# Performance work log

Measured on AMD Instinct MI355X. Metric: run time of the kernel, lower is better.

Reference implementation:

```python
import jax, jax.numpy as jnp
import numpy as np

MARGIN = 1.0
N, D = 4096, 512
NUM_CLASSES = 64


def setup_inputs() -> dict:
    key = jax.random.key(0)
    k1, k2 = jax.random.split(key)
    inputs = jax.random.normal(k1, (N, D), dtype=jnp.float32)
    targets = jax.random.randint(k2, (N,), 0, NUM_CLASSES, dtype=jnp.int64)
    return {"inputs": inputs, "targets": targets}


def reference(inputs, targets):
    n = inputs.shape[0]
    sq = jnp.sum(inputs * inputs, axis=1)  # [n]
    # squared Euclidean distances, clamped at 0 (matches relu in original)
    d2 = jnp.maximum(sq[:, None] + sq[None, :] - 2.0 * (inputs @ inputs.T), 0.0)
    # safe sqrt (zero entries get 0, matching forward; avoids NaN grads)
    dist = jnp.where(d2 > 0, jnp.sqrt(jnp.where(d2 > 0, d2, 1.0)), 0.0)  # [n,n]

    same = targets[:, None] == targets[None, :]
    eye = jnp.eye(n, dtype=bool)
    pos_mask = same & ~eye          # positives, diagonal excluded
    neg_mask = ~same                # negatives (diagonal is same-label, excluded)

    # per-row sum_k exp(margin - d_ik) over negatives  (replaces per-pair loop)
    neg_sum = jnp.sum(jnp.where(neg_mask, jnp.exp(MARGIN - dist), 0.0), axis=1)  # [n]

    # J_ij = log(neg_sum_i + neg_sum_j) + d_ij for positive pairs
    J = jnp.log(neg_sum[:, None] + neg_sum[None, :]) + dist
    triu_pos = jnp.triu(pos_mask)   # loop iterated over upper-triangular positives
    hinge2 = jnp.where(triu_pos, jax.nn.relu(J) ** 2, 0.0)

    # original divides by count of ALL positive entries (both triangles)
    len_p = jnp.sum(pos_mask).astype(jnp.float32)
    return jnp.sum(hinge2) / len_p
```

## Files before the change

### kernel.cpp

```cpp
#include <hip/hip_runtime.h>
#include <math.h>

#define NN 4096
#define DD 512
#define MARGINF 1.0f
#define NCLS 64
#define MAXM 160
#define TRI (MAXM * (MAXM - 1) / 2)
#define PBLK 32
#define NBLK2 (PBLK * (PBLK + 1) / 2)
#define NSLICE 4

typedef __attribute__((ext_vector_type(8))) short bf16x8;
typedef __attribute__((ext_vector_type(4))) float f32x4;

#define WS_SQ   0
#define WS_NS   4096
#define WS_LOSS 8192
#define WS_CTR  8193
#define WS_LENP 8194
#define WS_RK   8320
#define WS_MEM  12416
#define WS_XF   32768
#define WS_PD   1081344

__device__ __forceinline__ unsigned short f2bf(float f) {
    unsigned u = __float_as_uint(f);
    u += 0x7fffu + ((u >> 16) & 1u);
    return (unsigned short)(u >> 16);
}

__global__ __launch_bounds__(256) void prep_kernel(const float* __restrict__ X,
                                                   const int* __restrict__ tgt,
                                                   float* __restrict__ ws) {
    __shared__ int tg[NN];
    const int tid = threadIdx.x;
    for (int j = tid; j < NN; j += 256) tg[j] = tgt[j];

    const int wv = tid >> 6, lane = tid & 63;
    const int row = blockIdx.x * 4 + wv;
    const float4* xr = (const float4*)(X + (size_t)row * DD);
    float4 a = xr[2 * lane], b = xr[2 * lane + 1];
    float s = a.x * a.x + a.y * a.y + a.z * a.z + a.w * a.w
            + b.x * b.x + b.y * b.y + b.z * b.z + b.w * b.w;
#pragma unroll
    for (int off = 32; off; off >>= 1) s += __shfl_down(s, off, 64);

    ushort4 pa = {f2bf(a.x), f2bf(a.y), f2bf(a.z), f2bf(a.w)};
    ushort4 pb = {f2bf(b.x), f2bf(b.y), f2bf(b.z), f2bf(b.w)};
    const int r16 = row >> 4, m = row & 15;
    const int kb = lane >> 2, q = lane & 3;
    ushort4* dst = (ushort4*)((unsigned short*)(ws + WS_XF)
                              + ((size_t)(r16 * 16 + kb) * 64 + q * 16 + m) * 8);
    dst[0] = pa;
    dst[1] = pb;

    __syncthreads();
    const int myc = tg[row];
    int cnt = 0;
    for (int j = lane; j < row; j += 64) cnt += (tg[j] == myc) ? 1 : 0;
#pragma unroll
    for (int off = 32; off; off >>= 1) cnt += __shfl_down(cnt, off, 64);
    if (lane == 0) {
        ws[WS_SQ + row] = s;
        ws[WS_NS + row] = 0.0f;
        ((int*)(ws + WS_RK))[row] = cnt;
        if (cnt < MAXM) ((int*)(ws + WS_MEM))[myc * MAXM + cnt] = row;
    }
    if (blockIdx.x == 0 && tid == 0) {
        ws[WS_LOSS] = 0.0f;
        ((unsigned*)ws)[WS_CTR] = 0u;
        ws[WS_LENP] = 0.0f;
    }
}

__global__ __launch_bounds__(256, 3) void negsum_kernel(const int* __restrict__ tgt,
                                                        float* __restrict__ ws) {
    __shared__ unsigned short lds[3][16][512];
    const int bidx = (blockIdx.x & 7) * 66 + (blockIdx.x >> 3);
    int bj = (int)((sqrtf(8.0f * (float)bidx + 1.0f) - 1.0f) * 0.5f);
    while (bj * (bj + 1) / 2 > bidx) --bj;
    while ((bj + 1) * (bj + 2) / 2 <= bidx) ++bj;
    const int bi = bidx - bj * (bj + 1) / 2;
    const int i0 = bi * 128, j0 = bj * 128;

    const int tid = threadIdx.x;
    const int w = tid >> 6, lane = tid & 63;
    const int m_ = lane & 15, q = lane >> 4;
    const int wr = (w & 1) * 64, wc = (w >> 1) * 64;
    const unsigned short* Xf = (const unsigned short*)(ws + WS_XF);
    const int air0 = i0 >> 4, bjr0 = j0 >> 4;

    int fr16[4];
#pragma unroll
    for (int s = 0; s < 4; ++s) {
        const int f = w * 4 + s;
        fr16[s] = (f < 8) ? (air0 + f) : (bjr0 + (f - 8));
    }

#define DMA_CHUNK(kb_, buf_)                                                   \
    {                                                                          \
        _Pragma("unroll")                                                      \
        for (int s = 0; s < 4; ++s) {                                          \
            const unsigned short* gp =                                         \
                Xf + ((size_t)fr16[s] * 16 + (kb_)) * 512 + lane * 8;          \
            __builtin_amdgcn_global_load_lds(                                  \
                (const __attribute__((address_space(1))) int*)gp,              \
                (__attribute__((address_space(3))) int*)(&lds[buf_][w * 4 + s][0]), \
                16, 0, 0);                                                     \
        }                                                                      \
    }

    f32x4 acc[4][4] = {};

    DMA_CHUNK(0, 0)
    DMA_CHUNK(1, 1)
    asm volatile("s_waitcnt vmcnt(4)" ::: "memory");
    __builtin_amdgcn_s_barrier();

#pragma unroll
    for (int t = 0; t < 16; ++t) {
        const int cur = t % 3;
        if (t < 14) DMA_CHUNK(t + 2, (t + 2) % 3)
        bf16x8 af[4], bf[4];
#pragma unroll
        for (int u = 0; u < 4; ++u)
            af[u] = *(const bf16x8*)&lds[cur][(w & 1) * 4 + u][lane * 8];
#pragma unroll
        for (int v = 0; v < 4; ++v)
            bf[v] = *(const bf16x8*)&lds[cur][8 + (w >> 1) * 4 + v][lane * 8];
#pragma unroll
        for (int u = 0; u < 4; ++u)
#pragma unroll
            for (int v = 0; v < 4; ++v)
                acc[u][v] = __builtin_amdgcn_mfma_f32_16x16x32_bf16(
                    af[u], bf[v], acc[u][v], 0, 0, 0);
        if (t < 14) {
            asm volatile("s_waitcnt vmcnt(4)" ::: "memory");
            __builtin_amdgcn_s_barrier();
        } else if (t == 14) {
            asm volatile("s_waitcnt vmcnt(0)" ::: "memory");
            __builtin_amdgcn_s_barrier();
        }
    }
#undef DMA_CHUNK

    const float* sq = ws + WS_SQ;
    float* ns = ws + WS_NS;
    const int* rk = (const int*)(ws + WS_RK);
    float* posd = ws + WS_PD;
    float sjv[4]; int tjv[4], jv[4];
#pragma unroll
    for (int v = 0; v < 4; ++v) {
        int j = j0 + wc + v * 16 + m_;
        jv[v] = j;
        sjv[v] = sq[j];
        tjv[v] = tgt[j];
    }
    float colp[4] = {0.0f, 0.0f, 0.0f, 0.0f};
#pragma unroll
    for (int u = 0; u < 4; ++u) {
#pragma unroll
        for (int r = 0; r < 4; ++r) {
            const int i = i0 + wr + u * 16 + q * 4 + r;
            const float si = sq[i];
            const int ti = tgt[i];
            float rp = 0.0f;
#pragma unroll
            for (int v = 0; v < 4; ++v) {
                float d2 = si + sjv[v] - 2.0f * acc[u][v][r];
                float dist = d2 > 0.0f ? sqrtf(d2) : 0.0f;
                if (tjv[v] != ti) {
                    float e = __expf(MARGINF - dist);
                    rp += e;
                    colp[v] += e;
                } else if (i < jv[v]) {
                    int ra = rk[i], rb = rk[jv[v]];
                    if (ra < MAXM && rb < MAXM) {
                        int hi = ra > rb ? ra : rb;
                        int lo = ra > rb ? rb : ra;
                        posd[ti * TRI + hi * (hi - 1) / 2 + lo] = dist;
                    }
                }
            }
            rp += __shfl_xor(rp, 1, 64);
            rp += __shfl_xor(rp, 2, 64);
            rp += __shfl_xor(rp, 4, 64);
            rp += __shfl_xor(rp, 8, 64);
            if (m_ == 0) atomicAdd(&ns[i], rp);
        }
    }
    if (bi != bj) {
#pragma unroll
        for (int v = 0; v < 4; ++v) {
            float cp = colp[v];
            cp += __shfl_xor(cp, 16, 64);
            cp += __shfl_xor(cp, 32, 64);
            if (q == 0) atomicAdd(&ns[jv[v]], cp);
        }
    }
}

__global__ __launch_bounds__(256) void pair2_kernel(const int* __restrict__ tgt,
                                                    float* __restrict__ ws,
                                                    float* __restrict__ out) {
    __shared__ float wsum[4];
    __shared__ int csum[4];
    __shared__ bool last;
    const int c = blockIdx.x >> 2;
    const int sl = blockIdx.x & 3;
    const int tid = threadIdx.x;
    const int wv = tid >> 6, lane = tid & 63;

    int ccount = 0;
    for (int j = tid; j < NN; j += 256) ccount += (tgt[j] == c) ? 1 : 0;
#pragma unroll
    for (int off = 32; off; off >>= 1) ccount += __shfl_down(ccount, off, 64);
    if (lane == 0) csum[wv] = ccount;
    __syncthreads();
    int mc = csum[0] + csum[1] + csum[2] + csum[3];
    if (mc > MAXM) mc = MAXM;
    const int P = mc * (mc - 1) / 2;

    const int* mem = (const int*)(ws + WS_MEM) + c * MAXM;
    const float* pd = ws + WS_PD + c * TRI;
    const float* ns = ws + WS_NS;
    float lsum = 0.0f;
    for (int p = tid + sl * 256; p < P; p += 256 * NSLICE) {
        int b = (int)((1.0f + sqrtf(1.0f + 8.0f * (float)p)) * 0.5f);
        while (b * (b - 1) / 2 > p) --b;
        while ((b + 1) * b / 2 <= p) ++b;
        const int a = p - b * (b - 1) / 2;
        const float dist = pd[b * (b - 1) / 2 + a];
        const int i = mem[a], j = mem[b];
        float J = __logf(ns[i] + ns[j]) + dist;
        float h = fmaxf(J, 0.0f);
        lsum += h * h;
    }
#pragma unroll
    for (int off = 32; off; off >>= 1) lsum += __shfl_xor(lsum, off, 64);
    if (lane == 0) wsum[wv] = lsum;
    __syncthreads();
    if (tid == 0) {
        float s = wsum[0] + wsum[1] + wsum[2] + wsum[3];
        if (s != 0.0f) atomicAdd(&ws[WS_LOSS], s);
        if (sl == 0) atomicAdd(&ws[WS_LENP], (float)(mc * (mc - 1)));
        __threadfence();
        unsigned d = atomicAdd((unsigned*)ws + WS_CTR, 1u);
        last = (d == NCLS * NSLICE - 1);
    }
    __syncthreads();
    if (last && tid == 0) {
        float total = atomicAdd(&ws[WS_LOSS], 0.0f);
        float lp = atomicAdd(&ws[WS_LENP], 0.0f);
        out[0] = total / lp;
    }
}

extern "C" void kernel_launch(void* const* d_in, const int* in_sizes, int n_in,
                              void* d_out, int out_size, void* d_ws, size_t ws_size,
                              hipStream_t stream) {
    const float* X  = (const float*)d_in[0];
    const int*  tgt = (const int*)d_in[1];
    float* ws  = (float*)d_ws;
    float* out = (float*)d_out;

    hipLaunchKernelGGL(prep_kernel, dim3(NN / 4), dim3(256), 0, stream, X, tgt, ws);
    hipLaunchKernelGGL(negsum_kernel, dim3(NBLK2), dim3(256), 0, stream, tgt, ws);
    hipLaunchKernelGGL(pair2_kernel, dim3(NCLS * NSLICE), dim3(256), 0, stream, tgt, ws, out);
}
```

Before: 116.1 us.

## Shrink negsum tiles to 64x64 single-wave blocks without barriers

Replaces the 128x128 four-wave negsum blocks with 64x64 tiles, each computed by a single 64-lane wave. Each wave now loads its own A and B fragments into LDS and waits only on its own counters, so the workgroup barriers go away. The grid grows from 528 to 2080 triangular blocks to spread work across more CUs. The cost is less operand reuse per tile, so global and LDS traffic per FLOP roughly doubles, and there are more atomic partial-sum writes.

```diff
diff --git a/kernel.cpp b/kernel.cpp
--- a/kernel.cpp
+++ b/kernel.cpp
@@ -7,8 +7,7 @@
 #define NCLS 64
 #define MAXM 160
 #define TRI (MAXM * (MAXM - 1) / 2)
-#define PBLK 32
-#define NBLK2 (PBLK * (PBLK + 1) / 2)
+#define NBLK 2080
 #define NSLICE 4
 
 typedef __attribute__((ext_vector_type(8))) short bf16x8;
@@ -74,39 +73,34 @@
     }
 }
 
-__global__ __launch_bounds__(256, 3) void negsum_kernel(const int* __restrict__ tgt,
-                                                        float* __restrict__ ws) {
-    __shared__ unsigned short lds[3][16][512];
-    const int bidx = (blockIdx.x & 7) * 66 + (blockIdx.x >> 3);
+__global__ __launch_bounds__(64) void negsum_kernel(const int* __restrict__ tgt,
+                                                    float* __restrict__ ws) {
+    __shared__ unsigned short lds[3][8][512];
+    const int bidx = (blockIdx.x & 7) * 260 + (blockIdx.x >> 3);
     int bj = (int)((sqrtf(8.0f * (float)bidx + 1.0f) - 1.0f) * 0.5f);
     while (bj * (bj + 1) / 2 > bidx) --bj;
     while ((bj + 1) * (bj + 2) / 2 <= bidx) ++bj;
     const int bi = bidx - bj * (bj + 1) / 2;
-    const int i0 = bi * 128, j0 = bj * 128;
-
-    const int tid = threadIdx.x;
-    const int w = tid >> 6, lane = tid & 63;
+    const int i0 = bi * 64, j0 = bj * 64;
+
+    const int lane = threadIdx.x;
     const int m_ = lane & 15, q = lane >> 4;
-    const int wr = (w & 1) * 64, wc = (w >> 1) * 64;
     const unsigned short* Xf = (const unsigned short*)(ws + WS_XF);
     const int air0 = i0 >> 4, bjr0 = j0 >> 4;
 
-    int fr16[4];
-#pragma unroll
-    for (int s = 0; s < 4; ++s) {
-        const int f = w * 4 + s;
-        fr16[s] = (f < 8) ? (air0 + f) : (bjr0 + (f - 8));
-    }
+    int fr16[8];
+#pragma unroll
+    for (int s = 0; s < 8; ++s) fr16[s] = (s < 4) ? (air0 + s) : (bjr0 + (s - 4));
 
 #define DMA_CHUNK(kb_, buf_)                                                   \
     {                                                                          \
         _Pragma("unroll")                                                      \
-        for (int s = 0; s < 4; ++s) {                                          \
+        for (int s = 0; s < 8; ++s) {                                          \
             const unsigned short* gp =                                         \
                 Xf + ((size_t)fr16[s] * 16 + (kb_)) * 512 + lane * 8;          \
             __builtin_amdgcn_global_load_lds(                                  \
                 (const __attribute__((address_space(1))) int*)gp,              \
-                (__attribute__((address_space(3))) int*)(&lds[buf_][w * 4 + s][0]), \
+                (__attribute__((address_space(3))) int*)(&lds[buf_][s][0]),    \
                 16, 0, 0);                                                     \
         }                                                                      \
     }
@@ -115,8 +109,7 @@
 
     DMA_CHUNK(0, 0)
     DMA_CHUNK(1, 1)
-    asm volatile("s_waitcnt vmcnt(4)" ::: "memory");
-    __builtin_amdgcn_s_barrier();
+    asm volatile("s_waitcnt vmcnt(8)" ::: "memory");
 
 #pragma unroll
     for (int t = 0; t < 16; ++t) {
@@ -125,10 +118,10 @@
         bf16x8 af[4], bf[4];
 #pragma unroll
         for (int u = 0; u < 4; ++u)
-            af[u] = *(const bf16x8*)&lds[cur][(w & 1) * 4 + u][lane * 8];
+            af[u] = *(const bf16x8*)&lds[cur][u][lane * 8];
 #pragma unroll
         for (int v = 0; v < 4; ++v)
-            bf[v] = *(const bf16x8*)&lds[cur][8 + (w >> 1) * 4 + v][lane * 8];
+            bf[v] = *(const bf16x8*)&lds[cur][4 + v][lane * 8];
 #pragma unroll
         for (int u = 0; u < 4; ++u)
 #pragma unroll
@@ -136,11 +129,9 @@
                 acc[u][v] = __builtin_amdgcn_mfma_f32_16x16x32_bf16(
                     af[u], bf[v], acc[u][v], 0, 0, 0);
         if (t < 14) {
-            asm volatile("s_waitcnt vmcnt(4)" ::: "memory");
-            __builtin_amdgcn_s_barrier();
+            asm volatile("s_waitcnt vmcnt(8) lgkmcnt(0)" ::: "memory");
         } else if (t == 14) {
-            asm volatile("s_waitcnt vmcnt(0)" ::: "memory");
-            __builtin_amdgcn_s_barrier();
+            asm volatile("s_waitcnt vmcnt(0) lgkmcnt(0)" ::: "memory");
         }
     }
 #undef DMA_CHUNK
@@ -152,7 +143,7 @@
     float sjv[4]; int tjv[4], jv[4];
 #pragma unroll
     for (int v = 0; v < 4; ++v) {
-        int j = j0 + wc + v * 16 + m_;
+        int j = j0 + v * 16 + m_;
         jv[v] = j;
         sjv[v] = sq[j];
         tjv[v] = tgt[j];
@@ -162,7 +153,7 @@
     for (int u = 0; u < 4; ++u) {
 #pragma unroll
         for (int r = 0; r < 4; ++r) {
-            const int i = i0 + wr + u * 16 + q * 4 + r;
+            const int i = i0 + u * 16 + q * 4 + r;
             const float si = sq[i];
             const int ti = tgt[i];
             float rp = 0.0f;
@@ -266,6 +257,6 @@
     float* out = (float*)d_out;
 
     hipLaunchKernelGGL(prep_kernel, dim3(NN / 4), dim3(256), 0, stream, X, tgt, ws);
-    hipLaunchKernelGGL(negsum_kernel, dim3(NBLK2), dim3(256), 0, stream, tgt, ws);
+    hipLaunchKernelGGL(negsum_kernel, dim3(NBLK), dim3(64), 0, stream, tgt, ws);
     hipLaunchKernelGGL(pair2_kernel, dim3(NCLS * NSLICE), dim3(256), 0, stream, tgt, ws, out);
 }
```

After: 132.2 us. 1.14x slower.
